# Optimization experiments

Hardware: AMD Instinct MI355X
Metric: run time of the kernel (lower is better)

The kernel has to match this reference:

```python
import jax, jax.numpy as jnp
import numpy as np


def conv1d(x, w, b, pad):
    # x: [B, C_in, T], w: [C_out, C_in, K] -> [B, C_out, T]
    y = jax.lax.conv_general_dilated(x, w, window_strides=(1,), padding=[(pad, pad)],
                                     dimension_numbers=('NCH', 'OIH', 'NCH'))
    return y + b[None, :, None]


def setup_inputs() -> dict:
    key = jax.random.key(0)
    ks = jax.random.split(key, 16)
    B, T1, T2 = 32, 1600, 400
    n_mel, n_text, n_att = 80, 512, 80
    w = lambda k, sh: jax.random.normal(k, sh, jnp.float32) * 0.02
    return {
        'queries': jax.random.normal(ks[0], (B, n_mel, T1), jnp.float32),
        'keys': jax.random.normal(ks[1], (B, n_text, T2), jnp.float32),
        'attn_prior': jax.random.uniform(ks[2], (B, T1, T2), jnp.float32),
        'mask': jax.random.randint(ks[3], (B, T2, 1), 0, 2).astype(bool),
        # key_proj params
        'kw1': w(ks[4], (n_text * 2, n_text, 3)), 'kb1': jnp.zeros((n_text * 2,), jnp.float32),
        'kw2': w(ks[5], (n_att, n_text * 2, 1)), 'kb2': jnp.zeros((n_att,), jnp.float32),
        # query_proj params
        'qw1': w(ks[6], (n_mel * 2, n_mel, 3)), 'qb1': jnp.zeros((n_mel * 2,), jnp.float32),
        'qw2': w(ks[7], (n_mel, n_mel * 2, 1)), 'qb2': jnp.zeros((n_mel,), jnp.float32),
        'qw3': w(ks[8], (n_att, n_mel, 1)), 'qb3': jnp.zeros((n_att,), jnp.float32),
    }


def reference(queries, keys, attn_prior, mask, kw1, kb1, kw2, kb2, qw1, qb1, qw2, qb2, qw3, qb3):
    # projections
    k = jax.nn.relu(conv1d(keys, kw1, kb1, 1))
    k = conv1d(k, kw2, kb2, 0)                          # [B, n_att, T2]
    q = jax.nn.relu(conv1d(queries, qw1, qb1, 1))
    q = jax.nn.relu(conv1d(q, qw2, qb2, 0))
    q = conv1d(q, qw3, qb3, 0)                          # [B, n_att, T1]
    # Gaussian isotropic attention: -0.0005 * sum_c (q_c - k_c)^2,
    # expanded as ||q||^2 + ||k||^2 - 2 q.k to avoid the [B,C,T1,T2] intermediate.
    q2 = jnp.sum(q * q, axis=1)                         # [B, T1]
    k2 = jnp.sum(k * k, axis=1)                         # [B, T2]
    qk = jnp.einsum('bct,bcs->bts', q, k)               # [B, T1, T2]
    attn = -0.0005 * (q2[:, :, None] + k2[:, None, :] - 2.0 * qk)
    attn = attn[:, None]                                # [B, 1, T1, T2]
    attn = jax.nn.log_softmax(attn, axis=3) + jnp.log(attn_prior[:, None] + 1e-8)
    attn_logprob = attn                                 # pre-mask log-probs
    m = mask.transpose(0, 2, 1)[:, None]                # [B, 1, 1, T2]
    attn = jnp.where(m, -jnp.inf, attn)
    attn = jax.nn.softmax(attn, axis=3)
    return attn, attn_logprob
```

## Files before the change

### kernel.cpp

```cpp
#include <hip/hip_runtime.h>
#include <math.h>


typedef __attribute__((ext_vector_type(8))) short bf16x8;
typedef __attribute__((ext_vector_type(4))) float f32x4;

static __device__ __forceinline__ unsigned short f2bf(float f) {
    union { float f; unsigned u; } v; v.f = f;
    unsigned r = v.u + 0x7FFF + ((v.u >> 16) & 1);
    return (unsigned short)(r >> 16);
}
static __device__ __forceinline__ float bf2f(unsigned short h) {
    union { unsigned u; float f; } v; v.u = ((unsigned)h) << 16;
    return v.f;
}

#define GLOAD16(g, s) __builtin_amdgcn_global_load_lds( \
    (const __attribute__((address_space(1))) void*)(g), \
    (__attribute__((address_space(3))) void*)(s), 16, 0, 0)

static __device__ __forceinline__ void fill_w(
    const float* __restrict__ w, unsigned short* __restrict__ dst, int rem,
    int Cout, int Cin, int KTAP, int CoutAlloc, int CinPad)
{
    int d  = rem / (CoutAlloc * CinPad);
    int r2 = rem - d * (CoutAlloc * CinPad);
    int co = r2 / CinPad, ci = r2 - co * CinPad;
    float v = (co < Cout && ci < Cin) ? w[((size_t)co * Cin + ci) * KTAP + d] : 0.f;
    dst[rem] = f2bf(v);
}

#define S0 1572864
#define S1 (S0+131072)
#define S2 (S1+73728)
#define S3 (S2+20480)
#define S4 (S3+12288)
#define S5 (S4+66560)
#define S6 (S5+12480)
#define NKB 6656
#define NQB 4896
#define NFB ((S6+255)/256)

static __device__ __forceinline__ void transpose_body(
    const float* __restrict__ in, unsigned short* __restrict__ Xt,
    int C, int CinPad, int T, int Trow,
    int bx, int by, int bz, float s[32][33])
{
    int ci0 = by * 32, tr0 = bx * 32;
    int tx = threadIdx.x & 31, ty = threadIdx.x >> 5;
#pragma unroll
    for (int i = 0; i < 4; i++) {
        int c = ci0 + ty + 8 * i;
        int t_in = tr0 + tx - 1;
        float v = (c < C && t_in >= 0 && t_in < T)
                    ? in[((size_t)bz * C + c) * T + t_in] : 0.f;
        s[ty + 8 * i][tx] = v;
    }
    __syncthreads();
    if (threadIdx.x < 128) {
        int row = threadIdx.x >> 2;
        int cq  = (threadIdx.x & 3) * 8;
        int tr  = tr0 + row;
        if (tr < Trow) {
            unsigned short pk[8];
#pragma unroll
            for (int e = 0; e < 8; e++) pk[e] = f2bf(s[cq + e][row]);
            *(bf16x8*)&Xt[((size_t)bz * Trow + tr) * CinPad + ci0 + cq] =
                *(const bf16x8*)pk;
        }
    }
}

__global__ __launch_bounds__(256) void prep_all(
    const float* __restrict__ keys, const float* __restrict__ queries,
    const float* __restrict__ kw1, const float* __restrict__ kw2,
    const float* __restrict__ qw1, const float* __restrict__ qw2,
    const float* __restrict__ qw3,
    unsigned short* __restrict__ Xk, unsigned short* __restrict__ Xq,
    unsigned short* __restrict__ Wk1, unsigned short* __restrict__ Wk2,
    unsigned short* __restrict__ Wq1, unsigned short* __restrict__ Wq2,
    unsigned short* __restrict__ Wq3)
{
    __shared__ float s[32][33];
    int bxg = blockIdx.x;
    if (bxg < NKB) {
        int x = bxg % 13, y = (bxg / 13) & 15, z = bxg / (13 * 16);
        transpose_body(keys, Xk, 512, 512, 400, 404, x, y, z, s);
    } else if (bxg < NKB + NQB) {
        int b2 = bxg - NKB;
        int x = b2 % 51, y = (b2 / 51) % 3, z = b2 / 153;
        transpose_body(queries, Xq, 80, 96, 1600, 1604, x, y, z, s);
    } else {
        int idx = (bxg - NKB - NQB) * 256 + threadIdx.x;
        if (idx < S0)      fill_w(kw1, Wk1, idx,       1024, 512, 3, 1024, 512);
        else if (idx < S1) fill_w(kw2, Wk2, idx - S0,  80, 1024, 1, 128, 1024);
        else if (idx < S2) fill_w(qw1, Wq1, idx - S1,  160, 80, 3, 256, 96);
        else if (idx < S3) fill_w(qw2, Wq2, idx - S2,  80, 160, 1, 128, 160);
        else if (idx < S4) fill_w(qw3, Wq3, idx - S3,  80, 80, 1, 128, 96);
        else if (idx < S5) Xk[(size_t)12928 * 512 + (idx - S4)] = 0;
        else if (idx < S6) Xq[(size_t)51328 * 96  + (idx - S5)] = 0;
    }
}

__global__ __launch_bounds__(512) void conv1_both(
    const unsigned short* __restrict__ Wk1, const unsigned short* __restrict__ Xk,
    const float* __restrict__ kb1, unsigned short* __restrict__ K1t,
    const unsigned short* __restrict__ Wq1, const unsigned short* __restrict__ Xq,
    const float* __restrict__ qb1, unsigned short* __restrict__ Q1t)
{
    constexpr int TRW = 136;
    __shared__ unsigned short lds[24576];

    const int tid  = threadIdx.x;
    const int lane = tid & 63;
    const int wid  = tid >> 6;
    const int wm   = wid >> 2;
    const int wn   = wid & 3;

    const int bid = blockIdx.x;
    const unsigned short* Wbf; const unsigned short* Xt;
    const float* bias; unsigned short* out;
    int CinPad, CoutAlloc, Cout, Trow, Tout, OutStride, nCo, Nvalid, wgid;
    if (bid < 408) {
        int xcd = bid & 7, ix = bid >> 3;
        wgid = xcd * 51 + ix;
        Wbf = Wk1; Xt = Xk; bias = kb1; out = K1t;
        CinPad = 512; CoutAlloc = 1024; Cout = 1024; Trow = 404; Tout = 400;
        OutStride = 1024; nCo = 8; Nvalid = 12928;
    } else {
        int b2 = bid - 408;
        int xcd = b2 & 7, ix = b2 >> 3;
        wgid = (xcd < 2 ? xcd * 51 : 2 * 51 + (xcd - 2) * 50) + ix;
        Wbf = Wq1; Xt = Xq; bias = qb1; out = Q1t;
        CinPad = 96; CoutAlloc = 256; Cout = 160; Trow = 1604; Tout = 1600;
        OutStride = 160; nCo = 2; Nvalid = 51328;
    }
    const int co0 = (wgid % nCo) * 128;
    const int n0  = (wgid / nCo) * 256;

    const int lr = lane >> 2;
    const int fr = lane & 15;
    const int lc = (((lane & 3) ^ ((lr >> 1) & 3)) * 8);
    const int ko = (((lane >> 4) ^ ((fr >> 1) & 3)) * 8);

    const int nKc   = CinPad >> 5;
    const int nIter = 3 * nKc;

    f32x4 a4[4][4] = {};

    int scc = 0, sd = 0;
#define STAGE(B)                                                                  \
    {                                                                             \
        const unsigned short* asrc =                                              \
            Wbf + ((size_t)sd * CoutAlloc + co0 + wid * 16 + lr) * CinPad + scc * 32 + lc; \
        const unsigned short* bsrc =                                              \
            Xt + ((size_t)(n0 + sd) + wid * 32 + lr) * CinPad + scc * 32 + lc;    \
        unsigned short* Ab = lds + (B) * 12288;                                   \
        GLOAD16(asrc, &Ab[wid * 512]);                                            \
        GLOAD16(bsrc, &Ab[4096 + wid * 1024]);                                    \
        GLOAD16(bsrc + (size_t)16 * CinPad, &Ab[4096 + wid * 1024 + 512]);        \
        scc++; if (scc == nKc) { scc = 0; sd++; }                                 \
    }

#define COMPUTE(B)                                                                \
    {                                                                             \
        const unsigned short* Ab = lds + (B) * 12288;                             \
        const unsigned short* Bb = Ab + 4096;                                     \
        bf16x8 af[4], bfr[4];                                                     \
        _Pragma("unroll")                                                         \
        for (int mi = 0; mi < 4; mi++)                                            \
            af[mi] = *(const bf16x8*)&Ab[(wm * 64 + mi * 16 + fr) * 32 + ko];     \
        _Pragma("unroll")                                                         \
        for (int ni = 0; ni < 4; ni++)                                            \
            bfr[ni] = *(const bf16x8*)&Bb[(wn * 64 + ni * 16 + fr) * 32 + ko];    \
        _Pragma("unroll")                                                         \
        for (int mi = 0; mi < 4; mi++)                                            \
            _Pragma("unroll")                                                     \
            for (int ni = 0; ni < 4; ni++)                                        \
                a4[mi][ni] = __builtin_amdgcn_mfma_f32_16x16x32_bf16(             \
                    af[mi], bfr[ni], a4[mi][ni], 0, 0, 0);                        \
    }

    STAGE(0);
    STAGE(1);

    for (int t = 0; t < nIter; t++) {
        if (t < nIter - 1)
            asm volatile("s_waitcnt vmcnt(3)" ::: "memory");
        else
            asm volatile("s_waitcnt vmcnt(0)" ::: "memory");
        __builtin_amdgcn_s_barrier();
        COMPUTE(t & 1);
        __builtin_amdgcn_s_barrier();
        if (t + 2 < nIter) STAGE(t & 1);
    }
#undef STAGE
#undef COMPUTE

    __syncthreads();

    int cw = OutStride - co0; if (cw > 128) cw = 128;
#pragma unroll
    for (int p = 0; p < 4; p++) {
        if (wn == p) {
#pragma unroll
            for (int mi = 0; mi < 4; mi++) {
                int col = wm * 64 + mi * 16 + (lane >> 4) * 4;
#pragma unroll
                for (int ni = 0; ni < 4; ni++) {
                    int row = ni * 16 + fr;
                    unsigned short pk[4];
#pragma unroll
                    for (int r = 0; r < 4; r++) {
                        int co = co0 + col + r;
                        float v = 0.f;
                        if (co < Cout) v = fmaxf(a4[mi][ni][r] + bias[co], 0.f);
                        pk[r] = f2bf(v);
                    }
                    *(unsigned long long*)&lds[row * TRW + col] = *(unsigned long long*)pk;
                }
            }
        }
        __syncthreads();
        int row = tid >> 3;
        int c0  = (tid & 7) * 16;
        int n   = n0 + p * 64 + row;
        if (n < Nvalid && c0 < cw) {
            int b = n / Trow;
            int t = n - b * Trow;
            if (t < Tout) {
                unsigned short* dst = out + ((size_t)b * Tout + t) * OutStride + co0 + c0;
                *(bf16x8*)&dst[0] = *(const bf16x8*)&lds[row * TRW + c0];
                *(bf16x8*)&dst[8] = *(const bf16x8*)&lds[row * TRW + c0 + 8];
            }
        }
        __syncthreads();
    }
}

__global__ __launch_bounds__(256) void conv2_both(
    const unsigned short* __restrict__ Wk2, const unsigned short* __restrict__ K1t,
    const float* __restrict__ kb2, unsigned short* __restrict__ Kt,
    float* __restrict__ k2s,
    const unsigned short* __restrict__ W2, const unsigned short* __restrict__ W3,
    const float* __restrict__ b2, const float* __restrict__ b3,
    const unsigned short* __restrict__ Q1t, unsigned short* __restrict__ Qt)
{
    constexpr int LDW = 40, TRW = 136, X2W = 104;
    __shared__ unsigned short lds[23552];
    unsigned short* Al = lds;
    unsigned short* Bl = lds + 5120;

    const int tid  = threadIdx.x;
    const int lane = tid & 63;
    const int wid  = tid >> 6;
    const int wm   = wid >> 1;
    const int wn   = wid & 1;
    const int r0 = tid >> 2;
    const int r1 = r0 + 64;
    const int q0 = (tid & 3) * 8;
    const int fr = lane & 15;
    const int ko = (lane >> 4) * 8;

    if (blockIdx.x < 100) {
        const int n0 = blockIdx.x * 128;
        f32x4 acc[4][4] = {};

        bf16x8 ra0 = *(const bf16x8*)&Wk2[(size_t)r0 * 1024 + q0];
        bf16x8 ra1 = *(const bf16x8*)&Wk2[(size_t)r1 * 1024 + q0];
        bf16x8 rb0 = *(const bf16x8*)&K1t[(size_t)(n0 + r0) * 1024 + q0];
        bf16x8 rb1 = *(const bf16x8*)&K1t[(size_t)(n0 + r1) * 1024 + q0];

        for (int kk = 0; kk < 32; kk++) {
            __syncthreads();
            *(bf16x8*)&Al[r0 * LDW + q0] = ra0;
            *(bf16x8*)&Al[r1 * LDW + q0] = ra1;
            *(bf16x8*)&Bl[r0 * LDW + q0] = rb0;
            *(bf16x8*)&Bl[r1 * LDW + q0] = rb1;
            __syncthreads();

            if (kk < 31) {
                int ci0 = (kk + 1) * 32;
                ra0 = *(const bf16x8*)&Wk2[(size_t)r0 * 1024 + ci0 + q0];
                ra1 = *(const bf16x8*)&Wk2[(size_t)r1 * 1024 + ci0 + q0];
                rb0 = *(const bf16x8*)&K1t[(size_t)(n0 + r0) * 1024 + ci0 + q0];
                rb1 = *(const bf16x8*)&K1t[(size_t)(n0 + r1) * 1024 + ci0 + q0];
            }

            bf16x8 af[4], bfr[4];
#pragma unroll
            for (int mi = 0; mi < 4; mi++)
                af[mi] = *(const bf16x8*)&Al[(wm * 64 + mi * 16 + fr) * LDW + ko];
#pragma unroll
            for (int ni = 0; ni < 4; ni++)
                bfr[ni] = *(const bf16x8*)&Bl[(wn * 64 + ni * 16 + fr) * LDW + ko];
#pragma unroll
            for (int mi = 0; mi < 4; mi++)
#pragma unroll
                for (int ni = 0; ni < 4; ni++)
                    acc[mi][ni] = __builtin_amdgcn_mfma_f32_16x16x32_bf16(
                        af[mi], bfr[ni], acc[mi][ni], 0, 0, 0);
        }

#pragma unroll
        for (int p = 0; p < 2; p++) {
            __syncthreads();
            if (wn == p) {
#pragma unroll
                for (int mi = 0; mi < 4; mi++) {
                    int col = wm * 64 + mi * 16 + (lane >> 4) * 4;
#pragma unroll
                    for (int ni = 0; ni < 4; ni++) {
                        int row = ni * 16 + fr;
                        unsigned short pk[4];
#pragma unroll
                        for (int r = 0; r < 4; r++) {
                            int co = col + r;
                            float v = 0.f;
                            if (co < 80) v = acc[mi][ni][r] + kb2[co];
                            pk[r] = f2bf(v);
                        }
                        *(unsigned long long*)&lds[row * TRW + col] = *(unsigned long long*)pk;
                    }
                }
            }
            __syncthreads();
            int rr = tid >> 2;
            int c0 = (tid & 3) * 32;
            int n  = n0 + p * 64 + rr;
            unsigned short* dst = Kt + (size_t)n * 96;
            float s = 0.f;
#pragma unroll
            for (int c = c0; c < c0 + 32; c += 8) {
                if (c < 96) {
                    bf16x8 v = *(const bf16x8*)&lds[rr * TRW + c];
                    *(bf16x8*)&dst[c] = v;
#pragma unroll
                    for (int e = 0; e < 8; e++) {
                        float f = bf2f((unsigned short)v[e]);
                        s = fmaf(f, f, s);
                    }
                }
            }
            s += __shfl_xor(s, 1);
            s += __shfl_xor(s, 2);
            if ((tid & 3) == 0) k2s[n] = s;
        }
    } else {
        unsigned short* X2 = lds + 10240;
        const int n0 = (blockIdx.x - 100) * 128;

        f32x4 acc[4][4] = {};

        bf16x8 ra0 = *(const bf16x8*)&W2[(size_t)r0 * 160 + q0];
        bf16x8 ra1 = *(const bf16x8*)&W2[(size_t)r1 * 160 + q0];
        bf16x8 rb0 = *(const bf16x8*)&Q1t[(size_t)(n0 + r0) * 160 + q0];
        bf16x8 rb1 = *(const bf16x8*)&Q1t[(size_t)(n0 + r1) * 160 + q0];

        for (int kk = 0; kk < 5; kk++) {
            __syncthreads();
            *(bf16x8*)&Al[r0 * LDW + q0] = ra0;
            *(bf16x8*)&Al[r1 * LDW + q0] = ra1;
            *(bf16x8*)&Bl[r0 * LDW + q0] = rb0;
            *(bf16x8*)&Bl[r1 * LDW + q0] = rb1;
            __syncthreads();

            if (kk < 4) {
                int ci0 = (kk + 1) * 32;
                ra0 = *(const bf16x8*)&W2[(size_t)r0 * 160 + ci0 + q0];
                ra1 = *(const bf16x8*)&W2[(size_t)r1 * 160 + ci0 + q0];
                rb0 = *(const bf16x8*)&Q1t[(size_t)(n0 + r0) * 160 + ci0 + q0];
                rb1 = *(const bf16x8*)&Q1t[(size_t)(n0 + r1) * 160 + ci0 + q0];
            }

            bf16x8 af[4], bfr[4];
#pragma unroll
            for (int mi = 0; mi < 4; mi++)
                af[mi] = *(const bf16x8*)&Al[(wm * 64 + mi * 16 + fr) * LDW + ko];
#pragma unroll
            for (int ni = 0; ni < 4; ni++)
                bfr[ni] = *(const bf16x8*)&Bl[(wn * 64 + ni * 16 + fr) * LDW + ko];
#pragma unroll
            for (int mi = 0; mi < 4; mi++)
#pragma unroll
                for (int ni = 0; ni < 4; ni++)
                    acc[mi][ni] = __builtin_amdgcn_mfma_f32_16x16x32_bf16(
                        af[mi], bfr[ni], acc[mi][ni], 0, 0, 0);
        }

#pragma unroll
        for (int mi = 0; mi < 4; mi++) {
            int col = wm * 64 + mi * 16 + (lane >> 4) * 4;
            if (col >= 96) continue;
#pragma unroll
            for (int ni = 0; ni < 4; ni++) {
                int row = wn * 64 + ni * 16 + fr;
                unsigned short pk[4];
#pragma unroll
                for (int r = 0; r < 4; r++) {
                    int co = col + r;
                    float v = 0.f;
                    if (co < 80) v = fmaxf(acc[mi][ni][r] + b2[co], 0.f);
                    pk[r] = f2bf(v);
                }
                *(unsigned long long*)&X2[row * X2W + col] = *(unsigned long long*)pk;
            }
        }

#pragma unroll
        for (int mi = 0; mi < 4; mi++)
#pragma unroll
            for (int ni = 0; ni < 4; ni++)
                acc[mi][ni] = (f32x4){0.f, 0.f, 0.f, 0.f};

        ra0 = *(const bf16x8*)&W3[(size_t)r0 * 96 + q0];
        ra1 = *(const bf16x8*)&W3[(size_t)r1 * 96 + q0];

        for (int kk = 0; kk < 3; kk++) {
            __syncthreads();
            *(bf16x8*)&Al[r0 * LDW + q0] = ra0;
            *(bf16x8*)&Al[r1 * LDW + q0] = ra1;
            __syncthreads();

            if (kk < 2) {
                int ci0 = (kk + 1) * 32;
                ra0 = *(const bf16x8*)&W3[(size_t)r0 * 96 + ci0 + q0];
                ra1 = *(const bf16x8*)&W3[(size_t)r1 * 96 + ci0 + q0];
            }

            bf16x8 af[4], bfr[4];
#pragma unroll
            for (int mi = 0; mi < 4; mi++)
                af[mi] = *(const bf16x8*)&Al[(wm * 64 + mi * 16 + fr) * LDW + ko];
#pragma unroll
            for (int ni = 0; ni < 4; ni++)
                bfr[ni] = *(const bf16x8*)&X2[(wn * 64 + ni * 16 + fr) * X2W + kk * 32 + ko];
#pragma unroll
            for (int mi = 0; mi < 4; mi++)
#pragma unroll
                for (int ni = 0; ni < 4; ni++)
                    acc[mi][ni] = __builtin_amdgcn_mfma_f32_16x16x32_bf16(
                        af[mi], bfr[ni], acc[mi][ni], 0, 0, 0);
        }

#pragma unroll
        for (int p = 0; p < 2; p++) {
            __syncthreads();
            if (wn == p) {
#pragma unroll
                for (int mi = 0; mi < 4; mi++) {
                    int col = wm * 64 + mi * 16 + (lane >> 4) * 4;
#pragma unroll
                    for (int ni = 0; ni < 4; ni++) {
                        int row = ni * 16 + fr;
                        unsigned short pk[4];
#pragma unroll
                        for (int r = 0; r < 4; r++) {
                            int co = col + r;
                            float v = 0.f;
                            if (co < 80) v = acc[mi][ni][r] + b3[co];
                            pk[r] = f2bf(v);
                        }
                        *(unsigned long long*)&lds[row * TRW + col] = *(unsigned long long*)pk;
                    }
                }
            }
            __syncthreads();
            int rr = tid >> 2;
            int c0 = (tid & 3) * 32;
            int n  = n0 + p * 64 + rr;
            unsigned short* dst = Qt + (size_t)n * 96;
#pragma unroll
            for (int c = c0; c < c0 + 32; c += 8)
                if (c < 96)
                    *(bf16x8*)&dst[c] = *(const bf16x8*)&lds[rr * TRW + c];
        }
    }
}

#define SCW 404
__global__ __launch_bounds__(512) void attn_v2(
    const unsigned short* __restrict__ Kt,
    const unsigned short* __restrict__ Qt,
    const float* __restrict__ k2s,
    const float* __restrict__ prior, const int* __restrict__ mask,
    float* __restrict__ out_attn, float* __restrict__ out_lp)
{
    const int T1 = 1600, T2 = 400;
    __shared__ float Sc[32 * SCW];

    const int tid  = threadIdx.x;
    const int lane = tid & 63;
    const int wid  = tid >> 6;
    const int b    = blockIdx.y;
    const int t0   = blockIdx.x * 32;
    const int fr   = lane & 15;
    const int ko   = (lane >> 4) * 8;

    bf16x8 qf[2][3];
#pragma unroll
    for (int ts = 0; ts < 2; ts++)
#pragma unroll
        for (int kk = 0; kk < 3; kk++)
            qf[ts][kk] = *(const bf16x8*)&Qt[((size_t)b * T1 + t0 + ts * 16 + fr) * 96 + kk * 32 + ko];

    for (int st = wid; st < 25; st += 8) {
        f32x4 acc0 = {}, acc1 = {};
#pragma unroll
        for (int kk = 0; kk < 3; kk++) {
            bf16x8 kf = *(const bf16x8*)&Kt[((size_t)b * T2 + st * 16 + fr) * 96 + kk * 32 + ko];
            acc0 = __builtin_amdgcn_mfma_f32_16x16x32_bf16(kf, qf[0][kk], acc0, 0, 0, 0);
            acc1 = __builtin_amdgcn_mfma_f32_16x16x32_bf16(kf, qf[1][kk], acc1, 0, 0, 0);
        }
        int sbase = st * 16 + (lane >> 4) * 4;
        float4 kv = *(const float4*)&k2s[b * T2 + sbase];
        float4 w0, w1;
        w0.x = fmaf(1e-3f, acc0[0], -5e-4f * kv.x);
        w0.y = fmaf(1e-3f, acc0[1], -5e-4f * kv.y);
        w0.z = fmaf(1e-3f, acc0[2], -5e-4f * kv.z);
        w0.w = fmaf(1e-3f, acc0[3], -5e-4f * kv.w);
        w1.x = fmaf(1e-3f, acc1[0], -5e-4f * kv.x);
        w1.y = fmaf(1e-3f, acc1[1], -5e-4f * kv.y);
        w1.z = fmaf(1e-3f, acc1[2], -5e-4f * kv.z);
        w1.w = fmaf(1e-3f, acc1[3], -5e-4f * kv.w);
        *(float4*)&Sc[fr * SCW + sbase]        = w0;
        *(float4*)&Sc[(16 + fr) * SCW + sbase] = w1;
    }

    const int s0i = lane * 4;
    const int s1i = 256 + lane * 4;
    const bool has1 = (lane < 36);

    int4 mk0 = *(const int4*)&mask[b * T2 + s0i];
    int4 mk1 = has1 ? *(const int4*)&mask[b * T2 + s1i] : make_int4(1, 1, 1, 1);

    __syncthreads();

    for (int r = 0; r < 4; r++) {
        int tloc = wid * 4 + r;
        int t = t0 + tloc;

        float4 v0 = *(const float4*)&Sc[tloc * SCW + s0i];
        float4 v1;
        if (has1) v1 = *(const float4*)&Sc[tloc * SCW + s1i];
        else      v1 = make_float4(-INFINITY, -INFINITY, -INFINITY, -INFINITY);

        float m = fmaxf(fmaxf(fmaxf(v0.x, v0.y), fmaxf(v0.z, v0.w)),
                        fmaxf(fmaxf(v1.x, v1.y), fmaxf(v1.z, v1.w)));
#pragma unroll
        for (int o = 32; o >= 1; o >>= 1) m = fmaxf(m, __shfl_xor(m, o));

        float sum = __expf(v0.x - m) + __expf(v0.y - m) + __expf(v0.z - m) + __expf(v0.w - m)
                  + __expf(v1.x - m) + __expf(v1.y - m) + __expf(v1.z - m) + __expf(v1.w - m);
#pragma unroll
        for (int o = 32; o >= 1; o >>= 1) sum += __shfl_xor(sum, o);
        float lse = m + __logf(sum);

        const float* pr = prior + ((size_t)b * T1 + t) * T2;
        float* lpout = out_lp + ((size_t)b * T1 + t) * T2;
        float* atout = out_attn + ((size_t)b * T1 + t) * T2;

        float4 p0 = *(const float4*)&pr[s0i];
        float4 p1 = has1 ? *(const float4*)&pr[s1i] : make_float4(0, 0, 0, 0);

        float4 lp0, lp1;
        lp0.x = v0.x - lse + __logf(p0.x + 1e-8f);
        lp0.y = v0.y - lse + __logf(p0.y + 1e-8f);
        lp0.z = v0.z - lse + __logf(p0.z + 1e-8f);
        lp0.w = v0.w - lse + __logf(p0.w + 1e-8f);
        lp1.x = v1.x - lse + __logf(p1.x + 1e-8f);
        lp1.y = v1.y - lse + __logf(p1.y + 1e-8f);
        lp1.z = v1.z - lse + __logf(p1.z + 1e-8f);
        lp1.w = v1.w - lse + __logf(p1.w + 1e-8f);

        *(float4*)&lpout[s0i] = lp0;
        if (has1) *(float4*)&lpout[s1i] = lp1;

        float4 val0, val1;
        val0.x = mk0.x ? -INFINITY : lp0.x;
        val0.y = mk0.y ? -INFINITY : lp0.y;
        val0.z = mk0.z ? -INFINITY : lp0.z;
        val0.w = mk0.w ? -INFINITY : lp0.w;
        val1.x = mk1.x ? -INFINITY : lp1.x;
        val1.y = mk1.y ? -INFINITY : lp1.y;
        val1.z = mk1.z ? -INFINITY : lp1.z;
        val1.w = mk1.w ? -INFINITY : lp1.w;
        if (!has1) val1 = make_float4(-INFINITY, -INFINITY, -INFINITY, -INFINITY);

        float m2 = fmaxf(fmaxf(fmaxf(val0.x, val0.y), fmaxf(val0.z, val0.w)),
                         fmaxf(fmaxf(val1.x, val1.y), fmaxf(val1.z, val1.w)));
#pragma unroll
        for (int o = 32; o >= 1; o >>= 1) m2 = fmaxf(m2, __shfl_xor(m2, o));

        float4 e0, e1;
        e0.x = __expf(val0.x - m2); e0.y = __expf(val0.y - m2);
        e0.z = __expf(val0.z - m2); e0.w = __expf(val0.w - m2);
        e1.x = __expf(val1.x - m2); e1.y = __expf(val1.y - m2);
        e1.z = __expf(val1.z - m2); e1.w = __expf(val1.w - m2);
        float sum2 = e0.x + e0.y + e0.z + e0.w + e1.x + e1.y + e1.z + e1.w;
#pragma unroll
        for (int o = 32; o >= 1; o >>= 1) sum2 += __shfl_xor(sum2, o);
        float inv = 1.f / sum2;

        float4 a0, a1;
        a0.x = e0.x * inv; a0.y = e0.y * inv; a0.z = e0.z * inv; a0.w = e0.w * inv;
        a1.x = e1.x * inv; a1.y = e1.y * inv; a1.z = e1.z * inv; a1.w = e1.w * inv;
        *(float4*)&atout[s0i] = a0;
        if (has1) *(float4*)&atout[s1i] = a1;
    }
}

extern "C" void kernel_launch(void* const* d_in, const int* in_sizes, int n_in,
                              void* d_out, int out_size, void* d_ws, size_t ws_size,
                              hipStream_t stream)
{
    (void)in_sizes; (void)n_in; (void)out_size; (void)ws_size;

    const float* queries = (const float*)d_in[0];
    const float* keys    = (const float*)d_in[1];
    const float* prior   = (const float*)d_in[2];
    const int*   mask    = (const int*)d_in[3];
    const float* kw1     = (const float*)d_in[4];
    const float* kb1     = (const float*)d_in[5];
    const float* kw2     = (const float*)d_in[6];
    const float* kb2     = (const float*)d_in[7];
    const float* qw1     = (const float*)d_in[8];
    const float* qb1     = (const float*)d_in[9];
    const float* qw2     = (const float*)d_in[10];
    const float* qb2     = (const float*)d_in[11];
    const float* qw3     = (const float*)d_in[12];
    const float* qb3     = (const float*)d_in[13];

    unsigned short* U = (unsigned short*)d_ws;
    unsigned short* K1t = U;
    unsigned short* Q1t = U;
    unsigned short* Xk  = U + 13107200;
    unsigned short* Qt  = U + 13107200;
    unsigned short* Xq  = U + 19792896;
    unsigned short* Kt  = U + 24732864;
    unsigned short* Wk1 = U + 25961664;
    unsigned short* Wk2 = U + 27534528;
    unsigned short* Wq1 = U + 27665600;
    unsigned short* Wq2 = U + 27739328;
    unsigned short* Wq3 = U + 27759808;
    float*          k2s = (float*)(U + 27772096);

    float* out_attn = (float*)d_out;
    float* out_lp   = out_attn + (size_t)32 * 1600 * 400;

    prep_all<<<NKB + NQB + NFB, dim3(256), 0, stream>>>(
        keys, queries, kw1, kw2, qw1, qw2, qw3,
        Xk, Xq, Wk1, Wk2, Wq1, Wq2, Wq3);

    conv1_both<<<810, dim3(512), 0, stream>>>(
        Wk1, Xk, kb1, K1t, Wq1, Xq, qb1, Q1t);

    conv2_both<<<500, dim3(256), 0, stream>>>(
        Wk2, K1t, kb2, Kt, k2s, Wq2, Wq3, qb2, qb3, Q1t, Qt);

    attn_v2<<<dim3(50, 32), dim3(512), 0, stream>>>(
        Kt, Qt, k2s, prior, mask, out_attn, out_lp);
}
```

Baseline: 216.4 us.

## Load conv1 weight fragments straight into registers and shrink LDS staging

In conv1_both, the weight (A) operand no longer goes through LDS. Each wave now loads its MFMA A fragments directly from global memory into registers, double-buffered across two register sets. Only the activation (B) tiles stay in double-buffered LDS, which cuts the shared-memory footprint from 48KB to 32KB and removes the A-side LDS reads. The cost is that waves sharing the same rows fetch the same weights redundantly from global or cache, and the pipeline's waitcnt bookkeeping becomes more complex.

Result: slower. 316.8 us (+46.4%).

```diff
diff --git a/kernel.cpp b/kernel.cpp
--- a/kernel.cpp
+++ b/kernel.cpp
@@ -109,7 +109,7 @@
     const float* __restrict__ qb1, unsigned short* __restrict__ Q1t)
 {
     constexpr int TRW = 136;
-    __shared__ unsigned short lds[24576];
+    __shared__ unsigned short lds[16384];
 
     const int tid  = threadIdx.x;
     const int lane = tid & 63;
@@ -138,8 +138,9 @@
     const int co0 = (wgid % nCo) * 128;
     const int n0  = (wgid / nCo) * 256;
 
-    const int lr = lane >> 2;
-    const int fr = lane & 15;
+    const int lr  = lane >> 2;
+    const int fr  = lane & 15;
+    const int frk = (lane >> 4) * 8;
     const int lc = (((lane & 3) ^ ((lr >> 1) & 3)) * 8);
     const int ko = (((lane >> 4) ^ ((fr >> 1) & 3)) * 8);
 
@@ -147,29 +148,34 @@
     const int nIter = 3 * nKc;
 
     f32x4 a4[4][4] = {};
-
-    int scc = 0, sd = 0;
-#define STAGE(B)                                                                  \
+    bf16x8 paA[4], paB[4];
+
+    int sbc = 0, sbd = 0;
+    int pac = 0, pad = 0;
+
+#define STAGE_B(BUF)                                                              \
     {                                                                             \
-        const unsigned short* asrc =                                              \
-            Wbf + ((size_t)sd * CoutAlloc + co0 + wid * 16 + lr) * CinPad + scc * 32 + lc; \
         const unsigned short* bsrc =                                              \
-            Xt + ((size_t)(n0 + sd) + wid * 32 + lr) * CinPad + scc * 32 + lc;    \
-        unsigned short* Ab = lds + (B) * 12288;                                   \
-        GLOAD16(asrc, &Ab[wid * 512]);                                            \
-        GLOAD16(bsrc, &Ab[4096 + wid * 1024]);                                    \
-        GLOAD16(bsrc + (size_t)16 * CinPad, &Ab[4096 + wid * 1024 + 512]);        \
-        scc++; if (scc == nKc) { scc = 0; sd++; }                                 \
-    }
-
-#define COMPUTE(B)                                                                \
+            Xt + ((size_t)(n0 + sbd) + wid * 32 + lr) * CinPad + sbc * 32 + lc;   \
+        unsigned short* Bb = lds + (BUF) * 8192;                                  \
+        GLOAD16(bsrc, &Bb[wid * 1024]);                                           \
+        GLOAD16(bsrc + (size_t)16 * CinPad, &Bb[wid * 1024 + 512]);               \
+        sbc++; if (sbc == nKc) { sbc = 0; sbd++; }                                \
+    }
+
+#define PA_LOAD(PA)                                                               \
     {                                                                             \
-        const unsigned short* Ab = lds + (B) * 12288;                             \
-        const unsigned short* Bb = Ab + 4096;                                     \
-        bf16x8 af[4], bfr[4];                                                     \
         _Pragma("unroll")                                                         \
         for (int mi = 0; mi < 4; mi++)                                            \
-            af[mi] = *(const bf16x8*)&Ab[(wm * 64 + mi * 16 + fr) * 32 + ko];     \
+            PA[mi] = *(const bf16x8*)&Wbf[((size_t)pad * CoutAlloc + co0 +        \
+                wm * 64 + mi * 16 + fr) * CinPad + pac * 32 + frk];               \
+        pac++; if (pac == nKc) { pac = 0; pad++; }                                \
+    }
+
+#define COMPUTE(BUF, PA)                                                          \
+    {                                                                             \
+        const unsigned short* Bb = lds + (BUF) * 8192;                            \
+        bf16x8 bfr[4];                                                            \
         _Pragma("unroll")                                                         \
         for (int ni = 0; ni < 4; ni++)                                            \
             bfr[ni] = *(const bf16x8*)&Bb[(wn * 64 + ni * 16 + fr) * 32 + ko];    \
@@ -178,23 +184,40 @@
             _Pragma("unroll")                                                     \
             for (int ni = 0; ni < 4; ni++)                                        \
                 a4[mi][ni] = __builtin_amdgcn_mfma_f32_16x16x32_bf16(             \
-                    af[mi], bfr[ni], a4[mi][ni], 0, 0, 0);                        \
-    }
-
-    STAGE(0);
-    STAGE(1);
-
-    for (int t = 0; t < nIter; t++) {
-        if (t < nIter - 1)
-            asm volatile("s_waitcnt vmcnt(3)" ::: "memory");
+                    PA[mi], bfr[ni], a4[mi][ni], 0, 0, 0);                        \
+    }
+
+    STAGE_B(0);
+    STAGE_B(1);
+    PA_LOAD(paA);
+    asm volatile("s_waitcnt vmcnt(0)" ::: "memory");
+
+    int t = 0;
+    for (; t + 1 < nIter; t += 2) {
+        asm volatile("s_waitcnt vmcnt(2)" ::: "memory");
+        PA_LOAD(paB);
+        __builtin_amdgcn_s_barrier();
+        COMPUTE(0, paA);
+        __builtin_amdgcn_s_barrier();
+        if (t + 2 < nIter) STAGE_B(0);
+
+        if (t + 1 == nIter - 1)
+            asm volatile("s_waitcnt vmcnt(0)" ::: "memory");
         else
-            asm volatile("s_waitcnt vmcnt(0)" ::: "memory");
+            asm volatile("s_waitcnt vmcnt(2)" ::: "memory");
+        if (t + 2 < nIter) PA_LOAD(paA);
         __builtin_amdgcn_s_barrier();
-        COMPUTE(t & 1);
+        COMPUTE(1, paB);
         __builtin_amdgcn_s_barrier();
-        if (t + 2 < nIter) STAGE(t & 1);
-    }
-#undef STAGE
+        if (t + 3 < nIter) STAGE_B(1);
+    }
+    if (nIter & 1) {
+        asm volatile("s_waitcnt vmcnt(0)" ::: "memory");
+        __builtin_amdgcn_s_barrier();
+        COMPUTE(0, paA);
+    }
+#undef STAGE_B
+#undef PA_LOAD
 #undef COMPUTE
 
     __syncthreads();
@@ -227,9 +250,9 @@
         int n   = n0 + p * 64 + row;
         if (n < Nvalid && c0 < cw) {
             int b = n / Trow;
-            int t = n - b * Trow;
-            if (t < Tout) {
-                unsigned short* dst = out + ((size_t)b * Tout + t) * OutStride + co0 + c0;
+            int tt = n - b * Trow;
+            if (tt < Tout) {
+                unsigned short* dst = out + ((size_t)b * Tout + tt) * OutStride + co0 + c0;
                 *(bf16x8*)&dst[0] = *(const bf16x8*)&lds[row * TRW + c0];
                 *(bf16x8*)&dst[8] = *(const bf16x8*)&lds[row * TRW + c0 + 8];
             }
```

## Shrink conv1 tiles to 128x128 with 4 waves and triple-buffered loads

Applied to the files above, without the earlier changes.

The fused first-layer convolution kernel now uses 256-thread blocks computing 128x128 output tiles instead of 512-thread blocks with 128x256 tiles, which doubles the grid to 1610 blocks. The XCD-aware block-to-tile mapping is recomputed to match. The LDS ring goes from two buffers to three, so the next stage's global-to-LDS loads are issued before compute and each k-step needs only one barrier instead of two. The aim is better latency hiding and occupancy, at the cost of less operand reuse per block and more total weight reloads from global memory.

After: 234.3 us. 1.08x slower.

```diff
diff --git a/kernel.cpp b/kernel.cpp
--- a/kernel.cpp
+++ b/kernel.cpp
@@ -102,7 +102,7 @@
     }
 }
 
-__global__ __launch_bounds__(512) void conv1_both(
+__global__ __launch_bounds__(256) void conv1_both(
     const unsigned short* __restrict__ Wk1, const unsigned short* __restrict__ Xk,
     const float* __restrict__ kb1, unsigned short* __restrict__ K1t,
     const unsigned short* __restrict__ Wq1, const unsigned short* __restrict__ Xq,
@@ -114,29 +114,29 @@
     const int tid  = threadIdx.x;
     const int lane = tid & 63;
     const int wid  = tid >> 6;
-    const int wm   = wid >> 2;
-    const int wn   = wid & 3;
+    const int wm   = wid >> 1;
+    const int wn   = wid & 1;
 
     const int bid = blockIdx.x;
     const unsigned short* Wbf; const unsigned short* Xt;
     const float* bias; unsigned short* out;
-    int CinPad, CoutAlloc, Cout, Trow, Tout, OutStride, nCo, Nvalid, wgid;
-    if (bid < 408) {
+    int CinPad, CoutAlloc, Cout, Trow, Tout, OutStride, nCo, wgid;
+    if (bid < 808) {
         int xcd = bid & 7, ix = bid >> 3;
-        wgid = xcd * 51 + ix;
+        wgid = xcd * 101 + ix;
         Wbf = Wk1; Xt = Xk; bias = kb1; out = K1t;
         CinPad = 512; CoutAlloc = 1024; Cout = 1024; Trow = 404; Tout = 400;
-        OutStride = 1024; nCo = 8; Nvalid = 12928;
+        OutStride = 1024; nCo = 8;
     } else {
-        int b2 = bid - 408;
+        int b2 = bid - 808;
         int xcd = b2 & 7, ix = b2 >> 3;
-        wgid = (xcd < 2 ? xcd * 51 : 2 * 51 + (xcd - 2) * 50) + ix;
+        wgid = (xcd < 2 ? xcd * 101 : 202 + (xcd - 2) * 100) + ix;
         Wbf = Wq1; Xt = Xq; bias = qb1; out = Q1t;
         CinPad = 96; CoutAlloc = 256; Cout = 160; Trow = 1604; Tout = 1600;
-        OutStride = 160; nCo = 2; Nvalid = 51328;
+        OutStride = 160; nCo = 2;
     }
     const int co0 = (wgid % nCo) * 128;
-    const int n0  = (wgid / nCo) * 256;
+    const int n0  = (wgid / nCo) * 128;
 
     const int lr = lane >> 2;
     const int fr = lane & 15;
@@ -149,22 +149,23 @@
     f32x4 a4[4][4] = {};
 
     int scc = 0, sd = 0;
-#define STAGE(B)                                                                  \
+#define STAGE(BUF)                                                                \
     {                                                                             \
         const unsigned short* asrc =                                              \
-            Wbf + ((size_t)sd * CoutAlloc + co0 + wid * 16 + lr) * CinPad + scc * 32 + lc; \
+            Wbf + ((size_t)sd * CoutAlloc + co0 + wid * 32 + lr) * CinPad + scc * 32 + lc; \
         const unsigned short* bsrc =                                              \
             Xt + ((size_t)(n0 + sd) + wid * 32 + lr) * CinPad + scc * 32 + lc;    \
-        unsigned short* Ab = lds + (B) * 12288;                                   \
-        GLOAD16(asrc, &Ab[wid * 512]);                                            \
-        GLOAD16(bsrc, &Ab[4096 + wid * 1024]);                                    \
+        unsigned short* Ab = lds + (BUF) * 8192;                                  \
+        GLOAD16(asrc,                       &Ab[wid * 1024]);                     \
+        GLOAD16(asrc + (size_t)16 * CinPad, &Ab[wid * 1024 + 512]);               \
+        GLOAD16(bsrc,                       &Ab[4096 + wid * 1024]);              \
         GLOAD16(bsrc + (size_t)16 * CinPad, &Ab[4096 + wid * 1024 + 512]);        \
         scc++; if (scc == nKc) { scc = 0; sd++; }                                 \
     }
 
-#define COMPUTE(B)                                                                \
+#define COMPUTE(BUF)                                                              \
     {                                                                             \
-        const unsigned short* Ab = lds + (B) * 12288;                             \
+        const unsigned short* Ab = lds + (BUF) * 8192;                            \
         const unsigned short* Bb = Ab + 4096;                                     \
         bf16x8 af[4], bfr[4];                                                     \
         _Pragma("unroll")                                                         \
@@ -184,15 +185,16 @@
     STAGE(0);
     STAGE(1);
 
+    int b0 = 0, b1 = 1, b2c = 2;
     for (int t = 0; t < nIter; t++) {
         if (t < nIter - 1)
-            asm volatile("s_waitcnt vmcnt(3)" ::: "memory");
+            asm volatile("s_waitcnt vmcnt(4)" ::: "memory");
         else
             asm volatile("s_waitcnt vmcnt(0)" ::: "memory");
         __builtin_amdgcn_s_barrier();
-        COMPUTE(t & 1);
-        __builtin_amdgcn_s_barrier();
-        if (t + 2 < nIter) STAGE(t & 1);
+        if (t + 2 < nIter) STAGE(b2c);
+        COMPUTE(b0);
+        int tmp = b0; b0 = b1; b1 = b2c; b2c = tmp;
     }
 #undef STAGE
 #undef COMPUTE
@@ -201,7 +203,7 @@
 
     int cw = OutStride - co0; if (cw > 128) cw = 128;
 #pragma unroll
-    for (int p = 0; p < 4; p++) {
+    for (int p = 0; p < 2; p++) {
         if (wn == p) {
 #pragma unroll
             for (int mi = 0; mi < 4; mi++) {
@@ -222,17 +224,17 @@
             }
         }
         __syncthreads();
-        int row = tid >> 3;
-        int c0  = (tid & 7) * 16;
-        int n   = n0 + p * 64 + row;
-        if (n < Nvalid && c0 < cw) {
-            int b = n / Trow;
-            int t = n - b * Trow;
-            if (t < Tout) {
-                unsigned short* dst = out + ((size_t)b * Tout + t) * OutStride + co0 + c0;
-                *(bf16x8*)&dst[0] = *(const bf16x8*)&lds[row * TRW + c0];
-                *(bf16x8*)&dst[8] = *(const bf16x8*)&lds[row * TRW + c0 + 8];
-            }
+        int rr = tid >> 2;
+        int c0 = (tid & 3) * 32;
+        int n  = n0 + p * 64 + rr;
+        int b  = n / Trow;
+        int tt = n - b * Trow;
+        if (tt < Tout) {
+            unsigned short* dst = out + ((size_t)b * Tout + tt) * OutStride + co0;
+#pragma unroll
+            for (int c = c0; c < c0 + 32; c += 8)
+                if (c < cw)
+                    *(bf16x8*)&dst[c] = *(const bf16x8*)&lds[rr * TRW + c];
         }
         __syncthreads();
     }
@@ -652,7 +654,7 @@
         keys, queries, kw1, kw2, qw1, qw2, qw3,
         Xk, Xq, Wk1, Wk2, Wq1, Wq2, Wq3);
 
-    conv1_both<<<810, dim3(512), 0, stream>>>(
+    conv1_both<<<1610, dim3(256), 0, stream>>>(
         Wk1, Xk, kb1, K1t, Wq1, Xq, qb1, Q1t);
 
     conv2_both<<<500, dim3(256), 0, stream>>>(
```
